# Kernel tuning notes

Hardware: AMD Instinct MI355X
Metric: run time of the kernel (lower is better)

The kernel has to match this reference:

```python
import jax, jax.numpy as jnp
import numpy as np

N_NODES = 50000
N_EDGES = 800000
F_IN = 256
HID = 64
HEADS = 4
N_CLASSES = 2
N_GRAPHS = 512


def setup_inputs() -> dict:
    key = jax.random.key(0)
    ks = jax.random.split(key, 20)
    s = 0.05
    x = jax.random.normal(ks[0], (N_NODES, F_IN), jnp.float32)
    edge_index = jax.random.randint(ks[1], (2, N_EDGES), 0, N_NODES, jnp.int32)
    batch = jnp.sort(jax.random.randint(ks[2], (N_NODES,), 0, N_GRAPHS, jnp.int32))
    return {
        "x": x, "edge_index": edge_index, "batch": batch,
        # conv1: GATConv(F_IN, HID, heads=HEADS, concat=True)
        "W1": jax.random.normal(ks[3], (F_IN, HEADS * HID), jnp.float32) * s,
        "att_src1": jax.random.normal(ks[4], (HEADS, HID), jnp.float32) * s,
        "att_dst1": jax.random.normal(ks[5], (HEADS, HID), jnp.float32) * s,
        "b1": jnp.zeros((HEADS * HID,), jnp.float32),
        # conv2: GATConv(HEADS*HID, HID, heads=1, concat=False)
        "W2": jax.random.normal(ks[6], (HEADS * HID, HID), jnp.float32) * s,
        "att_src2": jax.random.normal(ks[7], (1, HID), jnp.float32) * s,
        "att_dst2": jax.random.normal(ks[8], (1, HID), jnp.float32) * s,
        "b2": jnp.zeros((HID,), jnp.float32),
        # global attention linear
        "Wg": jax.random.normal(ks[9], (HID, 1), jnp.float32) * s,
        "bg": jnp.zeros((1,), jnp.float32),
        # classifier
        "Wc1": jax.random.normal(ks[10], (HID, HID // 2), jnp.float32) * s,
        "bc1": jnp.zeros((HID // 2,), jnp.float32),
        "Wc2": jax.random.normal(ks[11], (HID // 2, N_CLASSES), jnp.float32) * s,
        "bc2": jnp.zeros((N_CLASSES,), jnp.float32),
    }


def _add_self_loops(edge_index, num_nodes):
    ar = jnp.arange(num_nodes, dtype=edge_index.dtype)
    return jnp.concatenate([edge_index, jnp.stack([ar, ar])], axis=1)


def _gat_conv(x, edge_index, W, a_src, a_dst, b, concat):
    # PyG GATConv (eval mode): h = xW, e = leaky_relu(a_s.h_src + a_d.h_dst),
    # alpha = segment_softmax(e, dst), out = scatter_add(alpha * h_src, dst)
    N = x.shape[0]
    H, C = a_src.shape
    h = (x @ W).reshape(N, H, C)                      # [N,H,C]
    src, dst = edge_index[0], edge_index[1]
    asrc = jnp.sum(h * a_src[None], axis=-1)          # [N,H]
    adst = jnp.sum(h * a_dst[None], axis=-1)          # [N,H]
    e = jax.nn.leaky_relu(asrc[src] + adst[dst], 0.2) # [E,H]
    emax = jax.ops.segment_max(e, dst, num_segments=N)
    e = jnp.exp(e - emax[dst])
    denom = jax.ops.segment_sum(e, dst, num_segments=N)
    alpha = e / (denom[dst] + 1e-16)                  # [E,H]
    msg = alpha[:, :, None] * h[src]                  # [E,H,C]
    out = jax.ops.segment_sum(msg, dst, num_segments=N)  # [N,H,C]
    out = out.reshape(N, H * C) if concat else out.mean(axis=1)
    return out + b


def _segment_softmax(v, seg, num_segments):
    m = jax.ops.segment_max(v, seg, num_segments=num_segments)
    e = jnp.exp(v - m[seg])
    s = jax.ops.segment_sum(e, seg, num_segments=num_segments)
    return e / (s[seg] + 1e-16)


def reference(x, edge_index, batch, W1, att_src1, att_dst1, b1,
              W2, att_src2, att_dst2, b2, Wg, bg, Wc1, bc1, Wc2, bc2):
    N = x.shape[0]
    ei = _add_self_loops(edge_index, N)
    h = _gat_conv(x, ei, W1, att_src1, att_dst1, b1, concat=True)
    h = jax.nn.elu(h)
    h = _gat_conv(h, ei, W2, att_src2, att_dst2, b2, concat=False)
    h = jax.nn.elu(h)                                  # [N,HID]
    att = (h @ Wg + bg)[:, 0]                          # [N]
    att = _segment_softmax(att, batch, N_GRAPHS)       # softmax over nodes per graph
    h = h * att[:, None]
    pooled = jax.ops.segment_sum(h, batch, num_segments=N_GRAPHS)  # [G,HID]
    hid = jax.nn.relu(pooled @ Wc1 + bc1)
    return hid @ Wc2 + bc2                             # [G, num_classes]
```

## Files before the change

### kernel.cpp

```cpp
#include <hip/hip_runtime.h>
#include <hip/hip_bf16.h>
#include <hip/hip_fp16.h>
#include <math.h>

#define N_NODES 50000
#define N_EDGES 800000
#define M_EDGES (N_EDGES + N_NODES)
#define NGRAPH 512

typedef __attribute__((ext_vector_type(8))) short bfrag8;
typedef __attribute__((ext_vector_type(4))) float floatx4;

__device__ __forceinline__ float wave_max(float v){
  #pragma unroll
  for (int o = 32; o; o >>= 1) v = fmaxf(v, __shfl_xor(v, o));
  return v;
}
__device__ __forceinline__ float wave_sum(float v){
  #pragma unroll
  for (int o = 32; o; o >>= 1) v += __shfl_xor(v, o);
  return v;
}
__device__ __forceinline__ unsigned short f2bf(float f){
  union { float f; unsigned int u; } v; v.f = f;
  unsigned int r = v.u + 0x7FFFu + ((v.u >> 16) & 1u);
  return (unsigned short)(r >> 16);
}
__device__ __forceinline__ float bf2f(unsigned short h){
  union { unsigned int u; float f; } v; v.u = ((unsigned int)h) << 16; return v.f;
}

__global__ void k_count(const int* __restrict__ ei, int* __restrict__ deg){
  int e = blockIdx.x * blockDim.x + threadIdx.x;
  if (e >= M_EDGES) return;
  int dst = (e < N_EDGES) ? ei[N_EDGES + e] : (e - N_EDGES);
  atomicAdd(&deg[dst], 1);
}

__global__ __launch_bounds__(1024) void k_scan(const int* __restrict__ deg,
                                               int* __restrict__ row_start){
  __shared__ int wsum[16];
  __shared__ int carry;
  const int tid = threadIdx.x, lane = tid & 63, wv = tid >> 6;
  if (tid == 0) carry = 0;
  __syncthreads();
  for (int b = 0; b < N_NODES; b += 1024){
    const int i = b + tid;
    const int v = (i < N_NODES) ? deg[i] : 0;
    int x = v;
    #pragma unroll
    for (int o = 1; o < 64; o <<= 1){
      int t = __shfl_up(x, o);
      if (lane >= o) x += t;
    }
    if (lane == 63) wsum[wv] = x;
    __syncthreads();
    if (tid == 0){
      int run = carry;
      #pragma unroll
      for (int k = 0; k < 16; ++k){ int t = wsum[k]; wsum[k] = run; run += t; }
      carry = run;
    }
    __syncthreads();
    if (i < N_NODES) row_start[i] = wsum[wv] + x - v;
    __syncthreads();
  }
}

__global__ void k_fill(const int* __restrict__ ei, const int* __restrict__ row_start,
                       int* __restrict__ fill, int* __restrict__ col){
  int e = blockIdx.x * blockDim.x + threadIdx.x;
  if (e >= M_EDGES) return;
  int src, dst;
  if (e < N_EDGES){ src = ei[e]; dst = ei[N_EDGES + e]; }
  else { src = dst = e - N_EDGES; }
  int slot = row_start[dst] + atomicAdd(&fill[dst], 1);
  col[slot] = src;
}

__global__ __launch_bounds__(768) void k_prep(const float* __restrict__ W1,
                                              const float* __restrict__ W2,
                                              const float* __restrict__ as1,
                                              const float* __restrict__ ad1,
                                              unsigned short* __restrict__ W1B3t,
                                              unsigned short* __restrict__ W2B3t,
                                              float* __restrict__ P){
  const int b = blockIdx.x, k = threadIdx.x;
  if (b < 256){
    float w = W1[(size_t)(k & 255) * 256 + b];
    unsigned short hi = f2bf(w);
    W1B3t[(size_t)b * 768 + k] = (k < 512) ? hi : f2bf(w - bf2f(hi));
  } else if (b < 320){
    int n = b - 256;
    float w = W2[(size_t)(k & 255) * 64 + n];
    unsigned short hi = f2bf(w);
    W2B3t[(size_t)n * 768 + k] = (k < 512) ? hi : f2bf(w - bf2f(hi));
  } else if (k < 256){
    float acc[8] = {0.f,0.f,0.f,0.f,0.f,0.f,0.f,0.f};
    for (int c = 0; c < 64; ++c){
      #pragma unroll
      for (int h = 0; h < 4; ++h){
        float w = W1[k * 256 + h * 64 + c];
        acc[h]     += w * as1[h * 64 + c];
        acc[4 + h] += w * ad1[h * 64 + c];
      }
    }
    #pragma unroll
    for (int j = 0; j < 8; ++j) P[k * 8 + j] = acc[j];
  }
}

__global__ __launch_bounds__(256) void k_att1p(const float* __restrict__ x,
                                               const float* __restrict__ P,
                                               float* __restrict__ asrc,
                                               float* __restrict__ adst,
                                               unsigned short* __restrict__ x2){
  __shared__ float Ps[256][9];
  const int tid = threadIdx.x;
  #pragma unroll
  for (int j = 0; j < 8; ++j) Ps[tid][j] = P[tid * 8 + j];
  __syncthreads();
  const int n = blockIdx.x * 4 + (tid >> 6);
  const int lane = tid & 63;
  float4 xv = *(const float4*)&x[(size_t)n * 256 + lane * 4];
  ushort4 hi4, lo4;
  hi4.x = f2bf(xv.x); lo4.x = f2bf(xv.x - bf2f(hi4.x));
  hi4.y = f2bf(xv.y); lo4.y = f2bf(xv.y - bf2f(hi4.y));
  hi4.z = f2bf(xv.z); lo4.z = f2bf(xv.z - bf2f(hi4.z));
  hi4.w = f2bf(xv.w); lo4.w = f2bf(xv.w - bf2f(hi4.w));
  *(ushort4*)&x2[(size_t)n * 512 + lane * 4] = hi4;
  *(ushort4*)&x2[(size_t)n * 512 + 256 + lane * 4] = lo4;
  float p[8];
  #pragma unroll
  for (int j = 0; j < 8; ++j){
    p[j] = xv.x * Ps[lane * 4 + 0][j] + xv.y * Ps[lane * 4 + 1][j]
         + xv.z * Ps[lane * 4 + 2][j] + xv.w * Ps[lane * 4 + 3][j];
    p[j] = wave_sum(p[j]);
  }
  if (lane == 0){
    *(float4*)&asrc[n * 4] = make_float4(p[0], p[1], p[2], p[3]);
    *(float4*)&adst[n * 4] = make_float4(p[4], p[5], p[6], p[7]);
  }
}

template<int BN, int OUT_HALF>
__global__ __launch_bounds__(256) void mfma_gemm(const unsigned short* __restrict__ A,
                                                 const unsigned short* __restrict__ Bt,
                                                 void* __restrict__ Cout,
                                                 int M, int ldc){
  __shared__ unsigned short As[128 * 64];
  __shared__ unsigned short Bs[BN * 64];
  const int tid = threadIdx.x;
  const int m0 = blockIdx.y * 128, n0 = blockIdx.x * BN;
  constexpr int NR = BN / 32;
  floatx4 acc[4][NR];
  #pragma unroll
  for (int mr = 0; mr < 4; ++mr)
    #pragma unroll
    for (int nr = 0; nr < NR; ++nr) acc[mr][nr] = (floatx4){0.f, 0.f, 0.f, 0.f};
  const int l = tid & 63, w = tid >> 6;
  const int wm = (w >> 1) * 64, wn = (w & 1) * (BN / 2);
  const int lr = l & 15;

  for (int kc = 0; kc < 768; kc += 64){
    #pragma unroll
    for (int i = 0; i < 4; ++i){
      int f = tid + i * 256, row = f >> 3, seg = f & 7;
      int sseg = seg ^ (row & 7);
      float4 v = make_float4(0.f, 0.f, 0.f, 0.f);
      if (m0 + row < M)
        v = *(const float4*)&A[(size_t)(m0 + row) * 512 + (kc & 511) + seg * 8];
      *(float4*)&As[row * 64 + sseg * 8] = v;
    }
    #pragma unroll
    for (int i = 0; i < BN / 32; ++i){
      int f = tid + i * 256, row = f >> 3, seg = f & 7;
      int sseg = seg ^ (row & 7);
      *(float4*)&Bs[row * 64 + sseg * 8] =
        *(const float4*)&Bt[(size_t)(n0 + row) * 768 + kc + seg * 8];
    }
    __syncthreads();
    #pragma unroll
    for (int kk = 0; kk < 2; ++kk){
      const int seg = kk * 4 + (l >> 4);
      bfrag8 bfr[NR];
      #pragma unroll
      for (int nr = 0; nr < NR; ++nr){
        const int br = wn + nr * 16 + lr;
        bfr[nr] = *(const bfrag8*)&Bs[br * 64 + (seg ^ (br & 7)) * 8];
      }
      #pragma unroll
      for (int mr = 0; mr < 4; ++mr){
        const int ar = wm + mr * 16 + lr;
        bfrag8 a = *(const bfrag8*)&As[ar * 64 + (seg ^ (ar & 7)) * 8];
        #pragma unroll
        for (int nr = 0; nr < NR; ++nr)
          acc[mr][nr] = __builtin_amdgcn_mfma_f32_16x16x32_bf16(a, bfr[nr], acc[mr][nr], 0, 0, 0);
      }
    }
    __syncthreads();
  }
  #pragma unroll
  for (int mr = 0; mr < 4; ++mr)
    #pragma unroll
    for (int nr = 0; nr < NR; ++nr){
      const int colg = n0 + wn + nr * 16 + lr;
      #pragma unroll
      for (int r = 0; r < 4; ++r){
        const int row = m0 + wm + mr * 16 + (l >> 4) * 4 + r;
        if (row < M){
          if (OUT_HALF)
            ((__half*)Cout)[(size_t)row * ldc + colg] = __float2half(acc[mr][nr][r]);
          else
            ((float*)Cout)[(size_t)row * ldc + colg] = acc[mr][nr][r];
        }
      }
    }
}

__global__ __launch_bounds__(256) void k_agg1w(const __half* __restrict__ h1,
                                               const int* __restrict__ col,
                                               const int* __restrict__ row_start,
                                               const int* __restrict__ degv,
                                               const float* __restrict__ asrc,
                                               const float* __restrict__ adst,
                                               const float* __restrict__ b1,
                                               unsigned short* __restrict__ out1s){
  const int tid = threadIdx.x, wv = tid >> 6, lane = tid & 63;
  const int n = blockIdx.x * 4 + wv;
  const int base = row_start[n], dg = degv[n];
  const float4 ad4 = *(const float4*)&adst[(size_t)n * 4];
  const int hsel = lane >> 4;
  float m0 = -3e38f, m1 = -3e38f, m2 = -3e38f, m3 = -3e38f;
  float s = 0.f;
  float4 acc = make_float4(0.f, 0.f, 0.f, 0.f);

  for (int c0 = 0; c0 < dg; c0 += 64){
    const int cnt = min(64, dg - c0);
    float e0 = -3e38f, e1 = -3e38f, e2 = -3e38f, e3 = -3e38f;
    int src = 0;
    if (lane < cnt){
      src = col[base + c0 + lane];
      const float4 s4 = *(const float4*)&asrc[(size_t)src * 4];
      e0 = s4.x + ad4.x; e0 = e0 > 0.f ? e0 : 0.2f * e0;
      e1 = s4.y + ad4.y; e1 = e1 > 0.f ? e1 : 0.2f * e1;
      e2 = s4.z + ad4.z; e2 = e2 > 0.f ? e2 : 0.2f * e2;
      e3 = s4.w + ad4.w; e3 = e3 > 0.f ? e3 : 0.2f * e3;
    }
    const float M0 = wave_max(e0), M1 = wave_max(e1), M2 = wave_max(e2), M3 = wave_max(e3);
    const float nm0 = fmaxf(m0, M0), nm1 = fmaxf(m1, M1);
    const float nm2 = fmaxf(m2, M2), nm3 = fmaxf(m3, M3);
    const float mo = hsel == 0 ? m0 : hsel == 1 ? m1 : hsel == 2 ? m2 : m3;
    const float mn = hsel == 0 ? nm0 : hsel == 1 ? nm1 : hsel == 2 ? nm2 : nm3;
    const float r = __expf(mo - mn);
    s *= r; acc.x *= r; acc.y *= r; acc.z *= r; acc.w *= r;
    m0 = nm0; m1 = nm1; m2 = nm2; m3 = nm3;
    const float w0 = __expf(e0 - nm0), w1 = __expf(e1 - nm1);
    const float w2 = __expf(e2 - nm2), w3 = __expf(e3 - nm3);
    const float S0 = wave_sum(w0), S1 = wave_sum(w1);
    const float S2 = wave_sum(w2), S3 = wave_sum(w3);
    s += hsel == 0 ? S0 : hsel == 1 ? S1 : hsel == 2 ? S2 : S3;
    int j = 0;
    for (; j + 4 <= cnt; j += 4){
      float wt[4]; int sj[4];
      #pragma unroll
      for (int u = 0; u < 4; ++u){
        const float t0 = __shfl(w0, j + u), t1 = __shfl(w1, j + u);
        const float t2 = __shfl(w2, j + u), t3 = __shfl(w3, j + u);
        wt[u] = hsel == 0 ? t0 : hsel == 1 ? t1 : hsel == 2 ? t2 : t3;
        sj[u] = __shfl(src, j + u);
      }
      uint2 rw[4];
      #pragma unroll
      for (int u = 0; u < 4; ++u)
        rw[u] = *(const uint2*)&h1[(size_t)sj[u] * 256 + lane * 4];
      #pragma unroll
      for (int u = 0; u < 4; ++u){
        float2 f01 = __half22float2(*reinterpret_cast<const __half2*>(&rw[u].x));
        float2 f23 = __half22float2(*reinterpret_cast<const __half2*>(&rw[u].y));
        acc.x += wt[u] * f01.x; acc.y += wt[u] * f01.y;
        acc.z += wt[u] * f23.x; acc.w += wt[u] * f23.y;
      }
    }
    for (; j < cnt; ++j){
      const float t0 = __shfl(w0, j), t1 = __shfl(w1, j);
      const float t2 = __shfl(w2, j), t3 = __shfl(w3, j);
      const float wt = hsel == 0 ? t0 : hsel == 1 ? t1 : hsel == 2 ? t2 : t3;
      const int sj = __shfl(src, j);
      const uint2 rw = *(const uint2*)&h1[(size_t)sj * 256 + lane * 4];
      float2 f01 = __half22float2(*reinterpret_cast<const __half2*>(&rw.x));
      float2 f23 = __half22float2(*reinterpret_cast<const __half2*>(&rw.y));
      acc.x += wt * f01.x; acc.y += wt * f01.y;
      acc.z += wt * f23.x; acc.w += wt * f23.y;
    }
  }
  const float inv = 1.f / (s + 1e-16f);
  const float4 bb = *(const float4*)&b1[lane * 4];
  float o0 = acc.x * inv + bb.x; o0 = o0 > 0.f ? o0 : __expf(o0) - 1.f;
  float o1 = acc.y * inv + bb.y; o1 = o1 > 0.f ? o1 : __expf(o1) - 1.f;
  float o2 = acc.z * inv + bb.z; o2 = o2 > 0.f ? o2 : __expf(o2) - 1.f;
  float o3 = acc.w * inv + bb.w; o3 = o3 > 0.f ? o3 : __expf(o3) - 1.f;
  ushort4 hi4, lo4;
  hi4.x = f2bf(o0); lo4.x = f2bf(o0 - bf2f(hi4.x));
  hi4.y = f2bf(o1); lo4.y = f2bf(o1 - bf2f(hi4.y));
  hi4.z = f2bf(o2); lo4.z = f2bf(o2 - bf2f(hi4.z));
  hi4.w = f2bf(o3); lo4.w = f2bf(o3 - bf2f(hi4.w));
  *(ushort4*)&out1s[(size_t)n * 512 + lane * 4] = hi4;
  *(ushort4*)&out1s[(size_t)n * 512 + 256 + lane * 4] = lo4;
}

__global__ __launch_bounds__(256) void k_att2(const __half* __restrict__ t2,
                                              const float* __restrict__ a_src,
                                              const float* __restrict__ a_dst,
                                              float* __restrict__ asrc,
                                              float* __restrict__ adst){
  const int tid = threadIdx.x, wv = tid >> 6, lane = tid & 63;
  const int n = blockIdx.x * 4 + wv;
  float v = __half2float(t2[(size_t)n * 64 + lane]);
  float ps = wave_sum(v * a_src[lane]);
  float pd = wave_sum(v * a_dst[lane]);
  if (lane == 0){ asrc[n] = ps; adst[n] = pd; }
}

__global__ __launch_bounds__(256) void k_agg2w(const __half* __restrict__ t2,
                                               const int* __restrict__ col,
                                               const int* __restrict__ row_start,
                                               const int* __restrict__ degv,
                                               const float* __restrict__ asrc,
                                               const float* __restrict__ adst,
                                               const float* __restrict__ b2,
                                               const float* __restrict__ Wg,
                                               const float* __restrict__ bg,
                                               float* __restrict__ hf,
                                               float* __restrict__ attg){
  const int tid = threadIdx.x, wv = tid >> 6, lane = tid & 63;
  const int n = blockIdx.x * 4 + wv;
  const int base = row_start[n], dg = degv[n];
  const float ad = adst[n];
  const int half = lane >> 5, c2 = lane & 31;
  float m = -3e38f, s = 0.f;
  float2 acc = make_float2(0.f, 0.f);

  for (int c0 = 0; c0 < dg; c0 += 64){
    const int cnt = min(64, dg - c0);
    float e = -3e38f; int src = 0;
    if (lane < cnt){
      src = col[base + c0 + lane];
      e = asrc[src] + ad;
      e = e > 0.f ? e : 0.2f * e;
    }
    const float M = wave_max(e);
    const float mn = fmaxf(m, M);
    const float r = __expf(m - mn);
    s *= r; acc.x *= r; acc.y *= r;
    m = mn;
    const float w = __expf(e - mn);
    s += wave_sum(w);
    for (int j = 0; j < cnt; j += 2){
      const int j0 = j + half;
      if (j0 < cnt){
        const float wt = __shfl(w, j0);
        const int sj = __shfl(src, j0);
        const unsigned int rw = *(const unsigned int*)&t2[(size_t)sj * 64 + c2 * 2];
        float2 f = __half22float2(*reinterpret_cast<const __half2*>(&rw));
        acc.x += wt * f.x; acc.y += wt * f.y;
      }
    }
  }
  acc.x += __shfl_xor(acc.x, 32);
  acc.y += __shfl_xor(acc.y, 32);
  const float inv = 1.f / (s + 1e-16f);
  float p = 0.f;
  if (half == 0){
    float o0 = acc.x * inv + b2[c2 * 2];     o0 = o0 > 0.f ? o0 : __expf(o0) - 1.f;
    float o1 = acc.y * inv + b2[c2 * 2 + 1]; o1 = o1 > 0.f ? o1 : __expf(o1) - 1.f;
    *(float2*)&hf[(size_t)n * 64 + c2 * 2] = make_float2(o0, o1);
    p = o0 * Wg[c2 * 2] + o1 * Wg[c2 * 2 + 1];
  }
  p = wave_sum(p);
  if (lane == 0) attg[n] = p + bg[0];
}

__global__ __launch_bounds__(256) void k_pool(const float* __restrict__ hf,
                                              const float* __restrict__ attg,
                                              const int* __restrict__ batch,
                                              const float* __restrict__ Wc1,
                                              const float* __restrict__ bc1,
                                              const float* __restrict__ Wc2,
                                              const float* __restrict__ bc2,
                                              float* __restrict__ out){
  __shared__ float redm[4], reds[4];
  __shared__ float pacc[4][64];
  __shared__ float pooled[64];
  __shared__ float hid[32];
  const int g = blockIdx.x, tid = threadIdx.x;
  const int wv = tid >> 6, lane = tid & 63;
  int lo = 0, hi = N_NODES;
  while (lo < hi){ int mid = (lo + hi) >> 1; if (batch[mid] < g) lo = mid + 1; else hi = mid; }
  const int s0 = lo;
  hi = N_NODES;
  while (lo < hi){ int mid = (lo + hi) >> 1; if (batch[mid] < g + 1) lo = mid + 1; else hi = mid; }
  const int s1 = lo;
  float lm = -3e38f;
  for (int j = s0 + tid; j < s1; j += 256) lm = fmaxf(lm, attg[j]);
  lm = wave_max(lm);
  if (lane == 0) redm[wv] = lm;
  __syncthreads();
  lm = fmaxf(fmaxf(redm[0], redm[1]), fmaxf(redm[2], redm[3]));
  float ls = 0.f;
  for (int j = s0 + tid; j < s1; j += 256) ls += __expf(attg[j] - lm);
  ls = wave_sum(ls);
  if (lane == 0) reds[wv] = ls;
  __syncthreads();
  ls = reds[0] + reds[1] + reds[2] + reds[3];
  const float inv = 1.f / (ls + 1e-16f);
  float acc = 0.f;
  for (int j = s0 + wv; j < s1; j += 4)
    acc += __expf(attg[j] - lm) * hf[(size_t)j * 64 + lane];
  pacc[wv][lane] = acc;
  __syncthreads();
  if (tid < 64)
    pooled[tid] = (pacc[0][tid] + pacc[1][tid] + pacc[2][tid] + pacc[3][tid]) * inv;
  __syncthreads();
  if (tid < 32){
    float t = bc1[tid];
    #pragma unroll
    for (int c = 0; c < 64; ++c) t += pooled[c] * Wc1[c * 32 + tid];
    hid[tid] = t > 0.f ? t : 0.f;
  }
  __syncthreads();
  if (tid < 2){
    float t = bc2[tid];
    #pragma unroll
    for (int c = 0; c < 32; ++c) t += hid[c] * Wc2[c * 2 + tid];
    out[g * 2 + tid] = t;
  }
}

extern "C" void kernel_launch(void* const* d_in, const int* in_sizes, int n_in,
                              void* d_out, int out_size, void* d_ws, size_t ws_size,
                              hipStream_t stream){
  const float* x    = (const float*)d_in[0];
  const int*   ei   = (const int*)d_in[1];
  const int*   batch= (const int*)d_in[2];
  const float* W1   = (const float*)d_in[3];
  const float* as1  = (const float*)d_in[4];
  const float* ad1  = (const float*)d_in[5];
  const float* b1   = (const float*)d_in[6];
  const float* W2   = (const float*)d_in[7];
  const float* as2  = (const float*)d_in[8];
  const float* ad2  = (const float*)d_in[9];
  const float* b2   = (const float*)d_in[10];
  const float* Wg   = (const float*)d_in[11];
  const float* bg   = (const float*)d_in[12];
  const float* Wc1  = (const float*)d_in[13];
  const float* bc1  = (const float*)d_in[14];
  const float* Wc2  = (const float*)d_in[15];
  const float* bc2  = (const float*)d_in[16];

  char* ws = (char*)d_ws;
  unsigned short* x2s   = (unsigned short*)(ws + 0LL);
  unsigned short* out1s = (unsigned short*)(ws + 0LL);
  __half* h1h   = (__half*)(ws + 51200000LL);
  __half* t2h   = (__half*)(ws + 102400000LL);
  float* hf     = (float*)(ws + 115200000LL);
  float* P      = (float*)(ws + 115200000LL);
  unsigned short* W1B3t = (unsigned short*)(ws + 115208192LL);
  unsigned short* W2B3t = (unsigned short*)(ws + 115601408LL);
  float* asrc1  = (float*)(ws + 128000000LL);
  float* adst1  = (float*)(ws + 128800000LL);
  float* asrc2  = (float*)(ws + 129600000LL);
  float* adst2  = (float*)(ws + 129800000LL);
  float* attg   = (float*)(ws + 130000000LL);
  int*   deg    = (int*)  (ws + 130200000LL);
  int*   fill   = (int*)  (ws + 130400000LL);
  int*   row_st = (int*)  (ws + 130600256LL);
  int*   col    = (int*)  (ws + 130800256LL);
  float* outf   = (float*)d_out;

  hipMemsetAsync(ws + 130200000LL, 0, 400256, stream);

  k_count<<<(M_EDGES + 255) / 256, 256, 0, stream>>>(ei, deg);
  k_scan<<<1, 1024, 0, stream>>>(deg, row_st);
  k_fill<<<(M_EDGES + 255) / 256, 256, 0, stream>>>(ei, row_st, fill, col);

  k_prep<<<321, 768, 0, stream>>>(W1, W2, as1, ad1, W1B3t, W2B3t, P);
  k_att1p<<<N_NODES / 4, 256, 0, stream>>>(x, P, asrc1, adst1, x2s);

  mfma_gemm<128, 1><<<dim3(2, 391), 256, 0, stream>>>(x2s, W1B3t, (void*)h1h, N_NODES, 256);
  k_agg1w<<<N_NODES / 4, 256, 0, stream>>>(h1h, col, row_st, deg, asrc1, adst1, b1, out1s);

  mfma_gemm<64, 1><<<dim3(1, 391), 256, 0, stream>>>(out1s, W2B3t, (void*)t2h, N_NODES, 64);
  k_att2<<<N_NODES / 4, 256, 0, stream>>>(t2h, as2, ad2, asrc2, adst2);
  k_agg2w<<<N_NODES / 4, 256, 0, stream>>>(t2h, col, row_st, deg, asrc2, adst2, b2, Wg, bg, hf, attg);

  k_pool<<<NGRAPH, 256, 0, stream>>>(hf, attg, batch, Wc1, bc1, Wc2, bc2, outf);
}
```

Baseline: 504.3 us.

## Merge CSR build kernels into neighbouring prep, attention and GEMM launches

The degree count is folded into the weight-prep kernel and the prefix scan into the attention/bf16-split kernel, where one extra block does a chunked scan. The CSR fill is appended as extra blocks of a dedicated first-layer MFMA GEMM kernel with a 1D grid. This cuts the launch count from 6 to 3 and lets the independent graph-structure work overlap with dense compute. The single-block scan of 50k entries runs serially per thread over chunks of 196 and may become a tail that delays the att kernel's completion.

```diff
diff --git a/kernel.cpp b/kernel.cpp
--- a/kernel.cpp
+++ b/kernel.cpp
@@ -30,72 +30,43 @@
   union { unsigned int u; float f; } v; v.u = ((unsigned int)h) << 16; return v.f;
 }
 
-__global__ void k_count(const int* __restrict__ ei, int* __restrict__ deg){
-  int e = blockIdx.x * blockDim.x + threadIdx.x;
-  if (e >= M_EDGES) return;
-  int dst = (e < N_EDGES) ? ei[N_EDGES + e] : (e - N_EDGES);
-  atomicAdd(&deg[dst], 1);
-}
-
-__global__ __launch_bounds__(1024) void k_scan(const int* __restrict__ deg,
-                                               int* __restrict__ row_start){
-  __shared__ int wsum[16];
-  __shared__ int carry;
-  const int tid = threadIdx.x, lane = tid & 63, wv = tid >> 6;
-  if (tid == 0) carry = 0;
-  __syncthreads();
-  for (int b = 0; b < N_NODES; b += 1024){
-    const int i = b + tid;
-    const int v = (i < N_NODES) ? deg[i] : 0;
-    int x = v;
-    #pragma unroll
-    for (int o = 1; o < 64; o <<= 1){
-      int t = __shfl_up(x, o);
-      if (lane >= o) x += t;
-    }
-    if (lane == 63) wsum[wv] = x;
-    __syncthreads();
-    if (tid == 0){
-      int run = carry;
-      #pragma unroll
-      for (int k = 0; k < 16; ++k){ int t = wsum[k]; wsum[k] = run; run += t; }
-      carry = run;
-    }
-    __syncthreads();
-    if (i < N_NODES) row_start[i] = wsum[wv] + x - v;
-    __syncthreads();
-  }
-}
-
-__global__ void k_fill(const int* __restrict__ ei, const int* __restrict__ row_start,
-                       int* __restrict__ fill, int* __restrict__ col){
-  int e = blockIdx.x * blockDim.x + threadIdx.x;
-  if (e >= M_EDGES) return;
-  int src, dst;
-  if (e < N_EDGES){ src = ei[e]; dst = ei[N_EDGES + e]; }
-  else { src = dst = e - N_EDGES; }
-  int slot = row_start[dst] + atomicAdd(&fill[dst], 1);
-  col[slot] = src;
-}
-
-__global__ __launch_bounds__(768) void k_prep(const float* __restrict__ W1,
-                                              const float* __restrict__ W2,
-                                              const float* __restrict__ as1,
-                                              const float* __restrict__ ad1,
-                                              unsigned short* __restrict__ W1B3t,
-                                              unsigned short* __restrict__ W2B3t,
-                                              float* __restrict__ P){
-  const int b = blockIdx.x, k = threadIdx.x;
-  if (b < 256){
-    float w = W1[(size_t)(k & 255) * 256 + b];
-    unsigned short hi = f2bf(w);
-    W1B3t[(size_t)b * 768 + k] = (k < 512) ? hi : f2bf(w - bf2f(hi));
-  } else if (b < 320){
-    int n = b - 256;
-    float w = W2[(size_t)(k & 255) * 64 + n];
-    unsigned short hi = f2bf(w);
-    W2B3t[(size_t)n * 768 + k] = (k < 512) ? hi : f2bf(w - bf2f(hi));
-  } else if (k < 256){
+#define NB_COUNT 3321
+__global__ __launch_bounds__(256) void k_prepc(const int* __restrict__ ei,
+                                               const float* __restrict__ W1,
+                                               const float* __restrict__ W2,
+                                               const float* __restrict__ as1,
+                                               const float* __restrict__ ad1,
+                                               int* __restrict__ deg,
+                                               unsigned short* __restrict__ W1B3t,
+                                               unsigned short* __restrict__ W2B3t,
+                                               float* __restrict__ P){
+  const int b = blockIdx.x, tid = threadIdx.x;
+  if (b < NB_COUNT){
+    int e = b * 256 + tid;
+    if (e < M_EDGES){
+      int dst = (e < N_EDGES) ? ei[N_EDGES + e] : (e - N_EDGES);
+      atomicAdd(&deg[dst], 1);
+    }
+  } else if (b < NB_COUNT + 256){
+    const int n = b - NB_COUNT;
+    #pragma unroll
+    for (int p = 0; p < 3; ++p){
+      const int k = p * 256 + tid;
+      float w = W1[(size_t)(k & 255) * 256 + n];
+      unsigned short hi = f2bf(w);
+      W1B3t[(size_t)n * 768 + k] = (k < 512) ? hi : f2bf(w - bf2f(hi));
+    }
+  } else if (b < NB_COUNT + 320){
+    const int n = b - (NB_COUNT + 256);
+    #pragma unroll
+    for (int p = 0; p < 3; ++p){
+      const int k = p * 256 + tid;
+      float w = W2[(size_t)(k & 255) * 64 + n];
+      unsigned short hi = f2bf(w);
+      W2B3t[(size_t)n * 768 + k] = (k < 512) ? hi : f2bf(w - bf2f(hi));
+    }
+  } else {
+    const int k = tid;
     float acc[8] = {0.f,0.f,0.f,0.f,0.f,0.f,0.f,0.f};
     for (int c = 0; c < 64; ++c){
       #pragma unroll
@@ -110,37 +81,143 @@
   }
 }
 
-__global__ __launch_bounds__(256) void k_att1p(const float* __restrict__ x,
+__global__ __launch_bounds__(256) void k_att1s(const float* __restrict__ x,
                                                const float* __restrict__ P,
                                                float* __restrict__ asrc,
                                                float* __restrict__ adst,
-                                               unsigned short* __restrict__ x2){
+                                               unsigned short* __restrict__ x2,
+                                               const int* __restrict__ deg,
+                                               int* __restrict__ row_start){
   __shared__ float Ps[256][9];
+  __shared__ int wsum[4];
   const int tid = threadIdx.x;
+  const int wv = tid >> 6, lane = tid & 63;
+  if (blockIdx.x < 12500){
+    #pragma unroll
+    for (int j = 0; j < 8; ++j) Ps[tid][j] = P[tid * 8 + j];
+    __syncthreads();
+    const int n = blockIdx.x * 4 + wv;
+    float4 xv = *(const float4*)&x[(size_t)n * 256 + lane * 4];
+    ushort4 hi4, lo4;
+    hi4.x = f2bf(xv.x); lo4.x = f2bf(xv.x - bf2f(hi4.x));
+    hi4.y = f2bf(xv.y); lo4.y = f2bf(xv.y - bf2f(hi4.y));
+    hi4.z = f2bf(xv.z); lo4.z = f2bf(xv.z - bf2f(hi4.z));
+    hi4.w = f2bf(xv.w); lo4.w = f2bf(xv.w - bf2f(hi4.w));
+    *(ushort4*)&x2[(size_t)n * 512 + lane * 4] = hi4;
+    *(ushort4*)&x2[(size_t)n * 512 + 256 + lane * 4] = lo4;
+    float p[8];
+    #pragma unroll
+    for (int j = 0; j < 8; ++j){
+      p[j] = xv.x * Ps[lane * 4 + 0][j] + xv.y * Ps[lane * 4 + 1][j]
+           + xv.z * Ps[lane * 4 + 2][j] + xv.w * Ps[lane * 4 + 3][j];
+      p[j] = wave_sum(p[j]);
+    }
+    if (lane == 0){
+      *(float4*)&asrc[n * 4] = make_float4(p[0], p[1], p[2], p[3]);
+      *(float4*)&adst[n * 4] = make_float4(p[4], p[5], p[6], p[7]);
+    }
+  } else {
+    const int CH = 196;
+    const int beg = tid * CH;
+    const int end = min(beg + CH, N_NODES);
+    int tot = 0;
+    for (int i = beg; i < end; ++i) tot += deg[i];
+    int xs = tot;
+    #pragma unroll
+    for (int o = 1; o < 64; o <<= 1){
+      int t = __shfl_up(xs, o);
+      if (lane >= o) xs += t;
+    }
+    if (lane == 63) wsum[wv] = xs;
+    __syncthreads();
+    int off = 0;
+    for (int k = 0; k < wv; ++k) off += wsum[k];
+    int run = off + xs - tot;
+    for (int i = beg; i < end; ++i){ row_start[i] = run; run += deg[i]; }
+  }
+}
+
+__global__ __launch_bounds__(256) void k_fg1(const unsigned short* __restrict__ A,
+                                             const unsigned short* __restrict__ Bt,
+                                             __half* __restrict__ C,
+                                             const int* __restrict__ ei,
+                                             const int* __restrict__ row_start,
+                                             int* __restrict__ fill,
+                                             int* __restrict__ col){
+  __shared__ unsigned short As[128 * 64];
+  __shared__ unsigned short Bs[128 * 64];
+  const int tid = threadIdx.x;
+  if (blockIdx.x >= 782){
+    int e = (blockIdx.x - 782) * 256 + tid;
+    if (e < M_EDGES){
+      int src, dst;
+      if (e < N_EDGES){ src = ei[e]; dst = ei[N_EDGES + e]; }
+      else { src = dst = e - N_EDGES; }
+      int slot = row_start[dst] + atomicAdd(&fill[dst], 1);
+      col[slot] = src;
+    }
+    return;
+  }
+  const int m0 = (blockIdx.x >> 1) * 128, n0 = (blockIdx.x & 1) * 128;
+  floatx4 acc[4][4];
   #pragma unroll
-  for (int j = 0; j < 8; ++j) Ps[tid][j] = P[tid * 8 + j];
-  __syncthreads();
-  const int n = blockIdx.x * 4 + (tid >> 6);
-  const int lane = tid & 63;
-  float4 xv = *(const float4*)&x[(size_t)n * 256 + lane * 4];
-  ushort4 hi4, lo4;
-  hi4.x = f2bf(xv.x); lo4.x = f2bf(xv.x - bf2f(hi4.x));
-  hi4.y = f2bf(xv.y); lo4.y = f2bf(xv.y - bf2f(hi4.y));
-  hi4.z = f2bf(xv.z); lo4.z = f2bf(xv.z - bf2f(hi4.z));
-  hi4.w = f2bf(xv.w); lo4.w = f2bf(xv.w - bf2f(hi4.w));
-  *(ushort4*)&x2[(size_t)n * 512 + lane * 4] = hi4;
-  *(ushort4*)&x2[(size_t)n * 512 + 256 + lane * 4] = lo4;
-  float p[8];
+  for (int mr = 0; mr < 4; ++mr)
+    #pragma unroll
+    for (int nr = 0; nr < 4; ++nr) acc[mr][nr] = (floatx4){0.f, 0.f, 0.f, 0.f};
+  const int l = tid & 63, w = tid >> 6;
+  const int wm = (w >> 1) * 64, wn = (w & 1) * 64;
+  const int lr = l & 15;
+
+  for (int kc = 0; kc < 768; kc += 64){
+    #pragma unroll
+    for (int i = 0; i < 4; ++i){
+      int f = tid + i * 256, row = f >> 3, seg = f & 7;
+      int sseg = seg ^ (row & 7);
+      float4 v = make_float4(0.f, 0.f, 0.f, 0.f);
+      if (m0 + row < N_NODES)
+        v = *(const float4*)&A[(size_t)(m0 + row) * 512 + (kc & 511) + seg * 8];
+      *(float4*)&As[row * 64 + sseg * 8] = v;
+    }
+    #pragma unroll
+    for (int i = 0; i < 4; ++i){
+      int f = tid + i * 256, row = f >> 3, seg = f & 7;
+      int sseg = seg ^ (row & 7);
+      *(float4*)&Bs[row * 64 + sseg * 8] =
+        *(const float4*)&Bt[(size_t)(n0 + row) * 768 + kc + seg * 8];
+    }
+    __syncthreads();
+    #pragma unroll
+    for (int kk = 0; kk < 2; ++kk){
+      const int seg = kk * 4 + (l >> 4);
+      bfrag8 bfr[4];
+      #pragma unroll
+      for (int nr = 0; nr < 4; ++nr){
+        const int br = wn + nr * 16 + lr;
+        bfr[nr] = *(const bfrag8*)&Bs[br * 64 + (seg ^ (br & 7)) * 8];
+      }
+      #pragma unroll
+      for (int mr = 0; mr < 4; ++mr){
+        const int ar = wm + mr * 16 + lr;
+        bfrag8 a = *(const bfrag8*)&As[ar * 64 + (seg ^ (ar & 7)) * 8];
+        #pragma unroll
+        for (int nr = 0; nr < 4; ++nr)
+          acc[mr][nr] = __builtin_amdgcn_mfma_f32_16x16x32_bf16(a, bfr[nr], acc[mr][nr], 0, 0, 0);
+      }
+    }
+    __syncthreads();
+  }
   #pragma unroll
-  for (int j = 0; j < 8; ++j){
-    p[j] = xv.x * Ps[lane * 4 + 0][j] + xv.y * Ps[lane * 4 + 1][j]
-         + xv.z * Ps[lane * 4 + 2][j] + xv.w * Ps[lane * 4 + 3][j];
-    p[j] = wave_sum(p[j]);
-  }
-  if (lane == 0){
-    *(float4*)&asrc[n * 4] = make_float4(p[0], p[1], p[2], p[3]);
-    *(float4*)&adst[n * 4] = make_float4(p[4], p[5], p[6], p[7]);
-  }
+  for (int mr = 0; mr < 4; ++mr)
+    #pragma unroll
+    for (int nr = 0; nr < 4; ++nr){
+      const int colg = n0 + wn + nr * 16 + lr;
+      #pragma unroll
+      for (int r = 0; r < 4; ++r){
+        const int row = m0 + wm + mr * 16 + (l >> 4) * 4 + r;
+        if (row < N_NODES)
+          C[(size_t)row * 256 + colg] = __float2half(acc[mr][nr][r]);
+      }
+    }
 }
 
 template<int BN, int OUT_HALF>
@@ -480,19 +557,12 @@
 
   hipMemsetAsync(ws + 130200000LL, 0, 400256, stream);
 
-  k_count<<<(M_EDGES + 255) / 256, 256, 0, stream>>>(ei, deg);
-  k_scan<<<1, 1024, 0, stream>>>(deg, row_st);
-  k_fill<<<(M_EDGES + 255) / 256, 256, 0, stream>>>(ei, row_st, fill, col);
-
-  k_prep<<<321, 768, 0, stream>>>(W1, W2, as1, ad1, W1B3t, W2B3t, P);
-  k_att1p<<<N_NODES / 4, 256, 0, stream>>>(x, P, asrc1, adst1, x2s);
-
-  mfma_gemm<128, 1><<<dim3(2, 391), 256, 0, stream>>>(x2s, W1B3t, (void*)h1h, N_NODES, 256);
+  k_prepc<<<NB_COUNT + 322, 256, 0, stream>>>(ei, W1, W2, as1, ad1, deg, W1B3t, W2B3t, P);
+  k_att1s<<<12501, 256, 0, stream>>>(x, P, asrc1, adst1, x2s, deg, row_st);
+  k_fg1<<<782 + NB_COUNT, 256, 0, stream>>>(x2s, W1B3t, h1h, ei, row_st, fill, col);
   k_agg1w<<<N_NODES / 4, 256, 0, stream>>>(h1h, col, row_st, deg, asrc1, adst1, b1, out1s);
-
   mfma_gemm<64, 1><<<dim3(1, 391), 256, 0, stream>>>(out1s, W2B3t, (void*)t2h, N_NODES, 64);
   k_att2<<<N_NODES / 4, 256, 0, stream>>>(t2h, as2, ad2, asrc2, adst2);
   k_agg2w<<<N_NODES / 4, 256, 0, stream>>>(t2h, col, row_st, deg, asrc2, adst2, b2, Wg, bg, hf, attg);
-
   k_pool<<<NGRAPH, 256, 0, stream>>>(hf, attg, batch, Wc1, bc1, Wc2, bc2, outf);
 }
```

After: 536.0 us. +6.3%, slower.
